# Kernel tuning notes

Hardware: AMD Instinct MI355X
Metric: run time of the kernel (lower is better)

Reference implementation:

```python
import jax, jax.numpy as jnp
import numpy as np

# Forest of complete L-ary trees, BFS level-contiguous node numbering.
B_TREES, ARITY, DEPTH = 8, 4, 8
C, M, NGEN = 8, 100, 4
COUNTS = [B_TREES * ARITY**l for l in range(DEPTH + 1)]
OFFS = np.concatenate([[0], np.cumsum(COUNTS)]).astype(np.int64)
DIM = int(OFFS[-1])  # 699048
# tree id of each node: within-level index // (ARITY**level)
BATCH = np.concatenate([np.arange(COUNTS[l]) // (ARITY**l) for l in range(DEPTH + 1)])


def setup_inputs() -> dict:
    key = jax.random.key(0)
    k1, k2, k3, k4 = jax.random.split(key, 4)
    return {
        "x": jax.random.randint(k1, (DIM,), 0, M, dtype=jnp.int32),
        "A": jax.random.normal(k2, (C, C, ARITY, NGEN), dtype=jnp.float32) * 2.5,
        "B_emit": jax.random.normal(k3, (C, M, NGEN), dtype=jnp.float32) * 2.5,
        "Pi": jax.random.normal(k4, (C, NGEN), dtype=jnp.float32) * 2.5,
    }


def _htmm_loglik(x, A, B_emit, Pi):
    # softmax reparameterization (matches F.softmax axes in torch code)
    smA = jax.nn.softmax(A, axis=0)            # [C,C,L,G], over child state
    smA_t = jnp.transpose(smA, (2, 0, 1, 3))   # [L,C,C,G]
    smB = jax.nn.softmax(B_emit, axis=1)       # [C,M,G]
    smPi = jax.nn.softmax(Pi, axis=0)          # [C,G]

    # preliminary downward: prior state distribution per node, level by level.
    # Children of a parent are contiguous with sibling position j = idx % ARITY.
    prior_lvls = [jnp.broadcast_to(smPi, (COUNTS[0], C, NGEN))]
    for l in range(1, DEPTH + 1):
        n_pa = COUNTS[l - 1]
        # prior_child[c] = sum_d A[c, d, pos_j, g] * prior_pa[d]
        pl = jnp.einsum('jcdg,pdg->pjcg', smA_t, prior_lvls[-1])
        prior_lvls.append(pl.reshape(n_pa * ARITY, C, NGEN))
    prior = jnp.concatenate(prior_lvls, axis=0)  # [DIM,C,G]

    em = jnp.transpose(smB[:, x], (1, 0, 2))     # [DIM,C,G]
    beta0 = prior * em

    ll = jnp.zeros((DIM, NGEN), dtype=beta0.dtype)
    # leaves = deepest level
    beta_lvl = beta0[OFFS[DEPTH]:OFFS[DEPTH + 1]]
    nu = beta_lvl.sum(1)                          # [n_leaves,G]
    beta_lvl = beta_lvl / nu[:, None, :]
    ll = ll.at[OFFS[DEPTH]:OFFS[DEPTH + 1]].set(jnp.log(nu))

    # upward recursion, bottom-up
    for l in range(DEPTH, 0, -1):
        n_pa = COUNTS[l - 1]
        ratio = (beta_lvl / prior[OFFS[l]:OFFS[l + 1]]).reshape(n_pa, ARITY, C, NGEN)
        # beta_uv[d] = sum_c A[c, d, pos_j, g] * beta_ch[c] / prior_ch[c]
        beta_uv = jnp.einsum('jcdg,pjcg->pjdg', smA_t, ratio)  # [n_pa,L,C,G]
        beta_pa = beta0[OFFS[l - 1]:OFFS[l]] * jnp.prod(beta_uv, axis=1)
        nu = beta_pa.sum(1)
        beta_lvl = beta_pa / nu[:, None, :]
        ll = ll.at[OFFS[l - 1]:OFFS[l]].set(jnp.log(nu))

    # scatter per-node log-likelihood contributions into per-tree totals
    return jax.ops.segment_sum(ll, jnp.asarray(BATCH), num_segments=B_TREES)  # [B_TREES,G]


def reference(x, A, B_emit, Pi):
    return _htmm_loglik(x, A, B_emit, Pi)
```

## Files before the change

### kernel.cpp

```cpp
#include <hip/hip_runtime.h>

constexpr int OFFS1 = 8, OFFS2 = 40, OFFS3 = 168, OFFS4 = 680;
constexpr int OFFS5 = 2728, OFFS6 = 10920, OFFS7 = 43688, OFFS8 = 174760;


#define AG_ST(p, v) __hip_atomic_store((p), (v), __ATOMIC_RELAXED, __HIP_MEMORY_SCOPE_AGENT)
#define AG_LD(p) __hip_atomic_load((p), __ATOMIC_RELAXED, __HIP_MEMORY_SCOPE_AGENT)

template <int CTRL>
static __device__ __forceinline__ float dppmov(float v) {
  return __int_as_float(__builtin_amdgcn_update_dpp(0, __float_as_int(v), CTRL, 0xF, 0xF, true));
}

static __device__ __forceinline__ float bfly8(float v) {
  v += dppmov<0xB1>(v);
  v += dppmov<0x4E>(v);
  v += dppmov<0x141>(v);
  return v;
}

static __device__ __forceinline__ void oct8(float v, float pv[8]) {
  float m = dppmov<0x141>(v);
  pv[0] = dppmov<0x00>(v); pv[1] = dppmov<0x55>(v);
  pv[2] = dppmov<0xAA>(v); pv[3] = dppmov<0xFF>(v);
  pv[4] = dppmov<0x00>(m); pv[5] = dppmov<0x55>(m);
  pv[6] = dppmov<0xAA>(m); pv[7] = dppmov<0xFF>(m);
}

static __device__ __forceinline__ float dot8(const float w[8], const float v[8]) {
  return w[0]*v[0] + w[1]*v[1] + w[2]*v[2] + w[3]*v[3] +
         w[4]*v[4] + w[5]*v[5] + w[6]*v[6] + w[7]*v[7];
}

static __device__ __forceinline__ void ld8(const float* p, float pv[8]) {
  const float4* q = (const float4*)p;
  float4 a = q[0], b = q[1];
  pv[0] = a.x; pv[1] = a.y; pv[2] = a.z; pv[3] = a.w;
  pv[4] = b.x; pv[5] = b.y; pv[6] = b.z; pv[7] = b.w;
}

static __device__ __forceinline__ void ld8p(const float* p, float wp[8], int h) {
  const float4* q = (const float4*)p;
  float4 a = q[h], b = q[1 - h];
  wp[0] = a.x; wp[1] = a.y; wp[2] = a.z; wp[3] = a.w;
  wp[4] = b.w; wp[5] = b.z; wp[6] = b.y; wp[7] = b.x;
}

static __device__ __forceinline__ float dot8p(const float wp[8], const float* p, int h) {
  const float4* q = (const float4*)p;
  float4 a = q[h], b = q[1 - h];
  return wp[0]*a.x + wp[1]*a.y + wp[2]*a.z + wp[3]*a.w +
         wp[4]*b.w + wp[5]*b.z + wp[6]*b.y + wp[7]*b.x;
}

static __device__ __forceinline__ float dot8r(const float w[8], const float* p) {
  const float4* q = (const float4*)p;
  float4 a = q[0], b = q[1];
  return w[0]*a.x + w[1]*a.y + w[2]*a.z + w[3]*a.w +
         w[4]*b.x + w[5]*b.y + w[6]*b.z + w[7]*b.w;
}

static __device__ __forceinline__ float rcpf(float x) { return __builtin_amdgcn_rcpf(x); }

static __device__ __forceinline__ float step_down(const float* wtd_l, float v, int j,
                                                  int r, int h) {
  const float* wb = &wtd_l[j * 256 + r];
  float w[8];
#pragma unroll
  for (int k = 0; k < 4; k++) {
    w[k]     = wb[(4 * h + k) * 32];
    w[4 + k] = wb[(7 - 4 * h - k) * 32];
  }
  float pv[8];
  oct8(v, pv);
  return dot8(w, pv);
}

__global__ __launch_bounds__(256) void k_all(const int* __restrict__ x,
                                             const float* __restrict__ A,
                                             const float* __restrict__ Bm,
                                             const float* __restrict__ Pi,
                                             float* __restrict__ RAT4,
                                             float* __restrict__ blocksum,
                                             unsigned* __restrict__ ctr,
                                             float* __restrict__ out) {
  __shared__ __align__(16) float wtd_l[1024];
  __shared__ __align__(16) float emt_l[3200];
  __shared__ __align__(16) float pit_l[32];
  __shared__ __align__(16) float etab_l[12800];
  __shared__ __align__(16) float shbuf[2304];
  __shared__ __align__(16) float rat5buf[16][32];
  __shared__ __align__(16) float pri4buf[4][32];
  __shared__ float llb[4];
  __shared__ int lastf;

  int t = threadIdx.x;
  int r = t & 31, g = r >> 3, s = r & 7, grp = t >> 5;
  int h = s >> 2;
  int b = blockIdx.x, tree = b >> 6;

  if (t < 128) {
    int d = t >> 4, j = (t >> 2) & 3, gg = t & 3;
    float v[8], sum = 0.f;
#pragma unroll
    for (int ss = 0; ss < 8; ss++) { v[ss] = __expf(A[((ss * 8 + d) * 4 + j) * 4 + gg]); sum += v[ss]; }
    float inv = rcpf(sum);
#pragma unroll
    for (int ss = 0; ss < 8; ss++) wtd_l[(j * 8 + d) * 32 + gg * 8 + ss] = v[ss] * inv;
  }
  if (t < 4) {
    float v[8], sum = 0.f;
#pragma unroll
    for (int c = 0; c < 8; c++) { v[c] = __expf(Pi[c * 4 + t]); sum += v[c]; }
    float inv = rcpf(sum);
#pragma unroll
    for (int c = 0; c < 8; c++) pit_l[t * 8 + c] = v[c] * inv;
    llb[t] = 0.f;
  }
  {
    int row = t >> 3, part = t & 7, c = row >> 2, gg = row & 3;
    int m0 = part < 4 ? part * 13 : 52 + (part - 4) * 12;
    int mn = part < 4 ? 13 : 12;
    float sum = 0.f;
    for (int m = m0; m < m0 + mn; m++) sum += __expf(Bm[(c * 100 + m) * 4 + gg]);
    sum = bfly8(sum);
    float inv = rcpf(sum);
    for (int m = m0; m < m0 + mn; m++)
      emt_l[m * 32 + gg * 8 + c] = __expf(Bm[(c * 100 + m) * 4 + gg]) * inv;
  }
  __syncthreads();
  {
    int c7 = t & 127, half = t >> 7;
    int j = c7 >> 5, d = (c7 >> 2) & 7, gg = c7 & 3;
    float w[8];
    ld8(&wtd_l[(j * 8 + d) * 32 + gg * 8], w);
    for (int m = half * 50; m < half * 50 + 50; m++)
      etab_l[(m * 4 + j) * 32 + gg * 8 + d] = dot8r(w, &emt_l[m * 32 + gg * 8]);
  }
  float wtd_p[4][8], wup_p[4][8];
#pragma unroll
  for (int j = 0; j < 4; j++) {
    const float* wb = &wtd_l[j * 256 + r];
#pragma unroll
    for (int k = 0; k < 4; k++) {
      wtd_p[j][k]     = wb[(4 * h + k) * 32];
      wtd_p[j][4 + k] = wb[(7 - 4 * h - k) * 32];
    }
    ld8p(&wtd_l[(j * 8 + s) * 32 + g * 8], wup_p[j], h);
  }
  __syncthreads();

  float acc = 0.f;
#pragma unroll 1
  for (int round = 0; round < 2; round++) {
    int n5 = b * 16 + round * 8 + grp;

    const int4* x8v = (const int4*)(x + OFFS8 + n5 * 64);
    const int4* x7p = (const int4*)(x + OFFS7 + n5 * 16);
    int4 x6v = *(const int4*)(x + OFFS6 + n5 * 4);
    int x5s = x[OFFS5 + n5];
    const int* x6a = (const int*)&x6v;
    int4 x7q[4];
#pragma unroll
    for (int q = 0; q < 4; q++) x7q[q] = x7p[q];
    int4 xls[4][4];
#pragma unroll
    for (int q = 0; q < 4; q++) xls[0][q] = x8v[q];

    float v5 = pit_l[r], pri4 = 0.f;
#pragma unroll
    for (int k = 1; k <= 5; k++) {
      int j = (n5 >> (2 * (5 - k))) & 3;
      v5 = step_down(wtd_l, v5, j, r, h);
      if (k == 4) pri4 = v5;
    }
    float pv5[8];
    oct8(v5, pv5);

    float rat6[4];
#pragma unroll
    for (int q6 = 0; q6 < 4; q6++) {
      if (q6 < 3) {
#pragma unroll
        for (int q = 0; q < 4; q++) xls[q6 + 1][q] = x8v[(q6 + 1) * 4 + q];
      }
      float u6 = dot8(wtd_p[q6], pv5);
      float pv6[8];
      oct8(u6, pv6);
      const int* x7a = (const int*)&x7q[q6];

      float Ep[4][4];
#pragma unroll
      for (int q7 = 0; q7 < 4; q7++) {
        const int* xla = (const int*)&xls[q6][q7];
#pragma unroll
        for (int j = 0; j < 4; j++) Ep[q7][j] = etab_l[(xla[j] * 4 + j) * 32 + r];
      }

      float rat7[4];
#pragma unroll
      for (int q7 = 0; q7 < 4; q7++) {
        float u7 = dot8(wtd_p[q7], pv6);
        float n0 = bfly8(u7 * Ep[q7][0]);
        float n1 = bfly8(u7 * Ep[q7][1]);
        float n2 = bfly8(u7 * Ep[q7][2]);
        float n3 = bfly8(u7 * Ep[q7][3]);
        float p01 = n0 * n1, p23 = n2 * n3;
        float prod = (Ep[q7][0] * Ep[q7][1] * rcpf(p01)) * (Ep[q7][2] * Ep[q7][3] * rcpf(p23));
        acc += __logf(p01) + __logf(p23);
        float em = emt_l[x7a[q7] * 32 + r];
        float nu7 = bfly8(u7 * em * prod);
        acc += __logf(nu7);
        rat7[q7] = em * prod * rcpf(nu7);
      }
      float prod6 = 1.f;
#pragma unroll
      for (int j = 0; j < 4; j++) {
        float pr[8];
        oct8(rat7[j], pr);
        prod6 *= dot8(wup_p[j], pr);
      }
      float em6 = emt_l[x6a[q6] * 32 + r];
      float nu6 = bfly8(u6 * em6 * prod6);
      acc += __logf(nu6);
      rat6[q6] = em6 * prod6 * rcpf(nu6);
    }
    {
      float prod5 = 1.f;
#pragma unroll
      for (int j = 0; j < 4; j++) {
        float pr[8];
        oct8(rat6[j], pr);
        prod5 *= dot8(wup_p[j], pr);
      }
      float em5 = emt_l[x5s * 32 + r];
      float nu5 = bfly8(v5 * em5 * prod5);
      acc += __logf(nu5);
      rat5buf[round * 8 + grp][r] = em5 * prod5 * rcpf(nu5);
    }
    if ((grp & 3) == 0) pri4buf[round * 2 + (grp >> 2)][r] = pri4;
  }
  __syncthreads();

  if (grp < 4) {
    int n4 = b * 4 + grp;
    float prod = 1.f;
#pragma unroll
    for (int j = 0; j < 4; j++) prod *= dot8p(wup_p[j], &rat5buf[grp * 4 + j][g * 8], h);
    float em = emt_l[x[OFFS4 + n4] * 32 + r];
    float pr4 = pri4buf[grp][r];
    float nu = bfly8(pr4 * em * prod);
    acc += __logf(nu);
    AG_ST(&RAT4[n4 * 32 + r], em * prod * rcpf(nu));
  }

  if (s == 0) atomicAdd(&llb[g], acc);
  __syncthreads();
  if (t < 4) AG_ST(&blocksum[b * 4 + t], llb[t]);
  asm volatile("s_waitcnt vmcnt(0)" ::: "memory");
  __syncthreads();
  if (t == 0) {
    unsigned old = __hip_atomic_fetch_add(&ctr[tree * 32], 1u, __ATOMIC_RELAXED,
                                          __HIP_MEMORY_SCOPE_AGENT);
    lastf = (old == 63u || old == 0xAAAAAAE9u) ? 1 : 0;
  }
  __syncthreads();
  if (!lastf) return;

  float* rat4_l = etab_l;
#pragma unroll
  for (int ib = 0; ib < 4; ib++) {
    float tmp[8];
#pragma unroll
    for (int i = 0; i < 8; i++) tmp[i] = AG_LD(&RAT4[tree * 8192 + (ib * 8 + i) * 256 + t]);
#pragma unroll
    for (int i = 0; i < 8; i++) rat4_l[(ib * 8 + i) * 256 + t] = tmp[i];
  }
  if (t < 4) llb[t] = 0.f;
  __syncthreads();

  float* st = &shbuf[grp * 288];
  float acc2 = 0.f;
#pragma unroll 1
  for (int ii = 0; ii < 2; ii++) {
    int l2 = ii * 8 + grp;
    int n2g = tree * 16 + l2;
    float v2 = pit_l[r];
    v2 = step_down(wtd_l, v2, (n2g >> 2) & 3, r, h);
    v2 = step_down(wtd_l, v2, n2g & 3, r, h);
    float pv2[8];
    oct8(v2, pv2);
    float rat3[4];
#pragma unroll
    for (int j3 = 0; j3 < 4; j3++) {
      int n3g = n2g * 4 + j3;
      int i3l = l2 * 4 + j3;
      float p3 = dot8(wtd_p[j3], pv2);
      float prod = 1.f;
#pragma unroll
      for (int j = 0; j < 4; j++) prod *= dot8p(wup_p[j], &rat4_l[(i3l * 4 + j) * 32 + g * 8], h);
      float em = emt_l[x[OFFS3 + n3g] * 32 + r];
      float nu = bfly8(p3 * em * prod);
      acc2 += __logf(nu);
      rat3[j3] = em * prod * rcpf(nu);
    }
    float prod = 1.f;
#pragma unroll
    for (int j = 0; j < 4; j++) {
      float pr[8];
      oct8(rat3[j], pr);
      prod *= dot8(wup_p[j], pr);
    }
    float em = emt_l[x[OFFS2 + n2g] * 32 + r];
    float nu = bfly8(v2 * em * prod);
    acc2 += __logf(nu);
    st[(5 + ii) * 32 + r] = em * prod * rcpf(nu);
  }
  __syncthreads();
  if (grp < 4) {
    int n1g = tree * 4 + grp;
    float pv[8];
    ld8(pit_l + g * 8, pv);
    float v1 = 0.f;
#pragma unroll
    for (int d = 0; d < 8; d++) v1 += wtd_l[(grp * 8 + d) * 32 + r] * pv[d];
    float prod = 1.f;
#pragma unroll
    for (int j = 0; j < 4; j++) {
      int l2 = grp * 4 + j;
      prod *= dot8p(wup_p[j], &shbuf[(l2 & 7) * 288 + (5 + (l2 >> 3)) * 32 + g * 8], h);
    }
    float em = emt_l[x[OFFS1 + n1g] * 32 + r];
    float nu = bfly8(v1 * em * prod);
    acc2 += __logf(nu);
    st[7 * 32 + r] = em * prod * rcpf(nu);
  }
  __syncthreads();
  if (grp == 0) {
    float pr = pit_l[r];
    float prod = 1.f;
#pragma unroll
    for (int j = 0; j < 4; j++) prod *= dot8p(wup_p[j], &shbuf[j * 288 + 7 * 32 + g * 8], h);
    float em = emt_l[x[tree] * 32 + r];
    float nu = bfly8(pr * em * prod);
    acc2 += __logf(nu);
  }
  __syncthreads();
  if (s == 0) atomicAdd(&llb[g], acc2);
  float v = AG_LD(&blocksum[tree * 256 + t]);
  __syncthreads();
  shbuf[t] = v;
  __syncthreads();
#pragma unroll
  for (int off = 128; off >= 4; off >>= 1) {
    if (t < off) shbuf[t] += shbuf[t + off];
    __syncthreads();
  }
  if (t < 4) out[tree * 4 + t] = shbuf[t] + llb[t];
}

extern "C" void kernel_launch(void* const* d_in, const int* in_sizes, int n_in,
                              void* d_out, int out_size, void* d_ws, size_t ws_size,
                              hipStream_t stream) {
  const int* x = (const int*)d_in[0];
  const float* A = (const float*)d_in[1];
  const float* Bm = (const float*)d_in[2];
  const float* Pi = (const float*)d_in[3];
  float* ws = (float*)d_ws;
  unsigned* ctr = (unsigned*)d_ws;
  float* blocksum = ws + 256;
  float* RAT4 = ws + 256 + 2048;
  float* out = (float*)d_out;

  k_all<<<512, 256, 0, stream>>>(x, A, Bm, Pi, RAT4, blocksum, ctr, out);
}
```

Measured before the change: 105.8 us.

## Shrink LDS footprint, drop precomputed emission table, double grid size

Removes the 12800-float etab table and computes leaf emission-transition products on the fly from emt_l. It also adds a transposed weight table so the preloaded wtd_p registers are no longer needed. With the smaller shared memory and launch_bounds(256,4), more blocks can be resident. The grid doubles to 1024 blocks, each handling one round of 8 level-5 subtrees, and the last-block reduction is adjusted to match (128 blocks per tree, two-phase staging of RAT4). The cost is extra per-leaf dot products in exchange for higher occupancy and parallelism.

```diff
diff --git a/kernel.cpp b/kernel.cpp
--- a/kernel.cpp
+++ b/kernel.cpp
@@ -32,13 +32,6 @@
          w[4]*v[4] + w[5]*v[5] + w[6]*v[6] + w[7]*v[7];
 }
 
-static __device__ __forceinline__ void ld8(const float* p, float pv[8]) {
-  const float4* q = (const float4*)p;
-  float4 a = q[0], b = q[1];
-  pv[0] = a.x; pv[1] = a.y; pv[2] = a.z; pv[3] = a.w;
-  pv[4] = b.x; pv[5] = b.y; pv[6] = b.z; pv[7] = b.w;
-}
-
 static __device__ __forceinline__ void ld8p(const float* p, float wp[8], int h) {
   const float4* q = (const float4*)p;
   float4 a = q[h], b = q[1 - h];
@@ -53,51 +46,61 @@
          wp[4]*b.w + wp[5]*b.z + wp[6]*b.y + wp[7]*b.x;
 }
 
-static __device__ __forceinline__ float dot8r(const float w[8], const float* p) {
-  const float4* q = (const float4*)p;
-  float4 a = q[0], b = q[1];
-  return w[0]*a.x + w[1]*a.y + w[2]*a.z + w[3]*a.w +
-         w[4]*b.x + w[5]*b.y + w[6]*b.z + w[7]*b.w;
-}
-
 static __device__ __forceinline__ float rcpf(float x) { return __builtin_amdgcn_rcpf(x); }
 
-static __device__ __forceinline__ float step_down(const float* wtd_l, float v, int j,
-                                                  int r, int h) {
-  const float* wb = &wtd_l[j * 256 + r];
-  float w[8];
-#pragma unroll
-  for (int k = 0; k < 4; k++) {
-    w[k]     = wb[(4 * h + k) * 32];
-    w[4 + k] = wb[(7 - 4 * h - k) * 32];
-  }
+static __device__ __forceinline__ float step_down(const float* wtdT, float v, int j,
+                                                  int sg, int h) {
   float pv[8];
   oct8(v, pv);
-  return dot8(w, pv);
-}
-
-__global__ __launch_bounds__(256) void k_all(const int* __restrict__ x,
-                                             const float* __restrict__ A,
-                                             const float* __restrict__ Bm,
-                                             const float* __restrict__ Pi,
-                                             float* __restrict__ RAT4,
-                                             float* __restrict__ blocksum,
-                                             unsigned* __restrict__ ctr,
-                                             float* __restrict__ out) {
+  return dot8p(pv, &wtdT[(j * 32 + sg) * 8], h);
+}
+
+static __device__ __forceinline__ float upprod(const float wup_p[4][8], const float rat[4]) {
+  float prod = 1.f;
+#pragma unroll
+  for (int j = 0; j < 4; j++) {
+    float pr[8];
+    oct8(rat[j], pr);
+    prod *= dot8(wup_p[j], pr);
+  }
+  return prod;
+}
+
+static __device__ __forceinline__ float leaf7(float u7, float e0, float e1, float e2,
+                                              float e3, float em, float* acc) {
+  float n0 = bfly8(u7 * e0), n1 = bfly8(u7 * e1);
+  float n2 = bfly8(u7 * e2), n3 = bfly8(u7 * e3);
+  float p01 = n0 * n1, p23 = n2 * n3;
+  float prod = (e0 * e1 * rcpf(p01)) * (e2 * e3 * rcpf(p23));
+  *acc += __logf(p01) + __logf(p23);
+  float nu7 = bfly8(u7 * em * prod);
+  *acc += __logf(nu7);
+  return em * prod * rcpf(nu7);
+}
+
+__global__ __launch_bounds__(256, 4) void k_all(const int* __restrict__ x,
+                                                const float* __restrict__ A,
+                                                const float* __restrict__ Bm,
+                                                const float* __restrict__ Pi,
+                                                float* __restrict__ RAT4,
+                                                float* __restrict__ blocksum,
+                                                unsigned* __restrict__ ctr,
+                                                float* __restrict__ out) {
   __shared__ __align__(16) float wtd_l[1024];
+  __shared__ __align__(16) float wtdT[1024];
   __shared__ __align__(16) float emt_l[3200];
   __shared__ __align__(16) float pit_l[32];
-  __shared__ __align__(16) float etab_l[12800];
-  __shared__ __align__(16) float shbuf[2304];
-  __shared__ __align__(16) float rat5buf[16][32];
-  __shared__ __align__(16) float pri4buf[4][32];
+  __shared__ __align__(16) float xb[640];
+  __shared__ __align__(16) float stg[4096];
   __shared__ float llb[4];
   __shared__ int lastf;
 
   int t = threadIdx.x;
   int r = t & 31, g = r >> 3, s = r & 7, grp = t >> 5;
   int h = s >> 2;
-  int b = blockIdx.x, tree = b >> 6;
+  int gb = g * 8;
+  int sg = s * 4 + g;
+  int b = blockIdx.x, tree = b >> 7;
 
   if (t < 128) {
     int d = t >> 4, j = (t >> 2) & 3, gg = t & 3;
@@ -129,49 +132,29 @@
       emt_l[m * 32 + gg * 8 + c] = __expf(Bm[(c * 100 + m) * 4 + gg]) * inv;
   }
   __syncthreads();
+  if (t < 128) {
+    int j = t >> 5, ss = (t >> 2) & 7, gg = t & 3;
+#pragma unroll
+    for (int d = 0; d < 8; d++) wtdT[t * 8 + d] = wtd_l[(j * 8 + d) * 32 + gg * 8 + ss];
+  }
+  float wup_p[4][8];
+#pragma unroll
+  for (int j = 0; j < 4; j++) ld8p(&wtd_l[(j * 8 + s) * 32 + gb], wup_p[j], h);
+  __syncthreads();
+
+  float acc = 0.f;
   {
-    int c7 = t & 127, half = t >> 7;
-    int j = c7 >> 5, d = (c7 >> 2) & 7, gg = c7 & 3;
-    float w[8];
-    ld8(&wtd_l[(j * 8 + d) * 32 + gg * 8], w);
-    for (int m = half * 50; m < half * 50 + 50; m++)
-      etab_l[(m * 4 + j) * 32 + gg * 8 + d] = dot8r(w, &emt_l[m * 32 + gg * 8]);
-  }
-  float wtd_p[4][8], wup_p[4][8];
-#pragma unroll
-  for (int j = 0; j < 4; j++) {
-    const float* wb = &wtd_l[j * 256 + r];
-#pragma unroll
-    for (int k = 0; k < 4; k++) {
-      wtd_p[j][k]     = wb[(4 * h + k) * 32];
-      wtd_p[j][4 + k] = wb[(7 - 4 * h - k) * 32];
-    }
-    ld8p(&wtd_l[(j * 8 + s) * 32 + g * 8], wup_p[j], h);
-  }
-  __syncthreads();
-
-  float acc = 0.f;
-#pragma unroll 1
-  for (int round = 0; round < 2; round++) {
-    int n5 = b * 16 + round * 8 + grp;
-
+    int n5 = b * 8 + grp;
     const int4* x8v = (const int4*)(x + OFFS8 + n5 * 64);
     const int4* x7p = (const int4*)(x + OFFS7 + n5 * 16);
     int4 x6v = *(const int4*)(x + OFFS6 + n5 * 4);
     int x5s = x[OFFS5 + n5];
     const int* x6a = (const int*)&x6v;
-    int4 x7q[4];
-#pragma unroll
-    for (int q = 0; q < 4; q++) x7q[q] = x7p[q];
-    int4 xls[4][4];
-#pragma unroll
-    for (int q = 0; q < 4; q++) xls[0][q] = x8v[q];
 
     float v5 = pit_l[r], pri4 = 0.f;
 #pragma unroll
     for (int k = 1; k <= 5; k++) {
-      int j = (n5 >> (2 * (5 - k))) & 3;
-      v5 = step_down(wtd_l, v5, j, r, h);
+      v5 = step_down(wtdT, v5, (n5 >> (2 * (5 - k))) & 3, sg, h);
       if (k == 4) pri4 = v5;
     }
     float pv5[8];
@@ -180,75 +163,45 @@
     float rat6[4];
 #pragma unroll
     for (int q6 = 0; q6 < 4; q6++) {
-      if (q6 < 3) {
-#pragma unroll
-        for (int q = 0; q < 4; q++) xls[q6 + 1][q] = x8v[(q6 + 1) * 4 + q];
-      }
-      float u6 = dot8(wtd_p[q6], pv5);
+      float u6 = dot8p(pv5, &wtdT[(q6 * 32 + sg) * 8], h);
       float pv6[8];
       oct8(u6, pv6);
-      const int* x7a = (const int*)&x7q[q6];
-
-      float Ep[4][4];
+      int4 x7q = x7p[q6];
+      const int* x7a = (const int*)&x7q;
+
+      float rat7[4];
 #pragma unroll
       for (int q7 = 0; q7 < 4; q7++) {
-        const int* xla = (const int*)&xls[q6][q7];
-#pragma unroll
-        for (int j = 0; j < 4; j++) Ep[q7][j] = etab_l[(xla[j] * 4 + j) * 32 + r];
+        int4 xl = x8v[q6 * 4 + q7];
+        const int* xa = (const int*)&xl;
+        float E[4];
+#pragma unroll
+        for (int j = 0; j < 4; j++) E[j] = dot8p(wup_p[j], &emt_l[xa[j] * 32 + gb], h);
+        float u7 = dot8p(pv6, &wtdT[(q7 * 32 + sg) * 8], h);
+        rat7[q7] = leaf7(u7, E[0], E[1], E[2], E[3], emt_l[x7a[q7] * 32 + r], &acc);
       }
-
-      float rat7[4];
-#pragma unroll
-      for (int q7 = 0; q7 < 4; q7++) {
-        float u7 = dot8(wtd_p[q7], pv6);
-        float n0 = bfly8(u7 * Ep[q7][0]);
-        float n1 = bfly8(u7 * Ep[q7][1]);
-        float n2 = bfly8(u7 * Ep[q7][2]);
-        float n3 = bfly8(u7 * Ep[q7][3]);
-        float p01 = n0 * n1, p23 = n2 * n3;
-        float prod = (Ep[q7][0] * Ep[q7][1] * rcpf(p01)) * (Ep[q7][2] * Ep[q7][3] * rcpf(p23));
-        acc += __logf(p01) + __logf(p23);
-        float em = emt_l[x7a[q7] * 32 + r];
-        float nu7 = bfly8(u7 * em * prod);
-        acc += __logf(nu7);
-        rat7[q7] = em * prod * rcpf(nu7);
-      }
-      float prod6 = 1.f;
-#pragma unroll
-      for (int j = 0; j < 4; j++) {
-        float pr[8];
-        oct8(rat7[j], pr);
-        prod6 *= dot8(wup_p[j], pr);
-      }
+      float prod6 = upprod(wup_p, rat7);
       float em6 = emt_l[x6a[q6] * 32 + r];
       float nu6 = bfly8(u6 * em6 * prod6);
       acc += __logf(nu6);
       rat6[q6] = em6 * prod6 * rcpf(nu6);
     }
-    {
-      float prod5 = 1.f;
-#pragma unroll
-      for (int j = 0; j < 4; j++) {
-        float pr[8];
-        oct8(rat6[j], pr);
-        prod5 *= dot8(wup_p[j], pr);
-      }
-      float em5 = emt_l[x5s * 32 + r];
-      float nu5 = bfly8(v5 * em5 * prod5);
-      acc += __logf(nu5);
-      rat5buf[round * 8 + grp][r] = em5 * prod5 * rcpf(nu5);
-    }
-    if ((grp & 3) == 0) pri4buf[round * 2 + (grp >> 2)][r] = pri4;
-  }
-  __syncthreads();
-
-  if (grp < 4) {
-    int n4 = b * 4 + grp;
+    float prod5 = upprod(wup_p, rat6);
+    float em5 = emt_l[x5s * 32 + r];
+    float nu5 = bfly8(v5 * em5 * prod5);
+    acc += __logf(nu5);
+    xb[grp * 32 + r] = em5 * prod5 * rcpf(nu5);
+    if ((grp & 3) == 0) xb[256 + (grp >> 2) * 32 + r] = pri4;
+  }
+  __syncthreads();
+
+  if (grp < 2) {
+    int n4 = b * 2 + grp;
     float prod = 1.f;
 #pragma unroll
-    for (int j = 0; j < 4; j++) prod *= dot8p(wup_p[j], &rat5buf[grp * 4 + j][g * 8], h);
+    for (int j = 0; j < 4; j++) prod *= dot8p(wup_p[j], &xb[(grp * 4 + j) * 32 + gb], h);
     float em = emt_l[x[OFFS4 + n4] * 32 + r];
-    float pr4 = pri4buf[grp][r];
+    float pr4 = xb[256 + grp * 32 + r];
     float nu = bfly8(pr4 * em * prod);
     acc += __logf(nu);
     AG_ST(&RAT4[n4 * 32 + r], em * prod * rcpf(nu));
@@ -262,101 +215,118 @@
   if (t == 0) {
     unsigned old = __hip_atomic_fetch_add(&ctr[tree * 32], 1u, __ATOMIC_RELAXED,
                                           __HIP_MEMORY_SCOPE_AGENT);
-    lastf = (old == 63u || old == 0xAAAAAAE9u) ? 1 : 0;
+    lastf = (old == 127u || old == 0xAAAAAB29u) ? 1 : 0;
   }
   __syncthreads();
   if (!lastf) return;
 
-  float* rat4_l = etab_l;
-#pragma unroll
-  for (int ib = 0; ib < 4; ib++) {
-    float tmp[8];
-#pragma unroll
-    for (int i = 0; i < 8; i++) tmp[i] = AG_LD(&RAT4[tree * 8192 + (ib * 8 + i) * 256 + t]);
-#pragma unroll
-    for (int i = 0; i < 8; i++) rat4_l[(ib * 8 + i) * 256 + t] = tmp[i];
-  }
+  float tmpA[16], tmpB[16];
+#pragma unroll
+  for (int i = 0; i < 16; i++) tmpA[i] = AG_LD(&RAT4[tree * 8192 + i * 256 + t]);
+#pragma unroll
+  for (int i = 0; i < 16; i++) stg[i * 256 + t] = tmpA[i];
+#pragma unroll
+  for (int i = 0; i < 16; i++) tmpB[i] = AG_LD(&RAT4[tree * 8192 + 4096 + i * 256 + t]);
   if (t < 4) llb[t] = 0.f;
   __syncthreads();
 
-  float* st = &shbuf[grp * 288];
   float acc2 = 0.f;
-#pragma unroll 1
-  for (int ii = 0; ii < 2; ii++) {
-    int l2 = ii * 8 + grp;
-    int n2g = tree * 16 + l2;
+  {
+    int n2A = tree * 16 + grp;
+    int4 x3A = *(const int4*)(x + OFFS3 + n2A * 4);
+    int x2A = x[OFFS2 + n2A];
+    const int* xa = (const int*)&x3A;
     float v2 = pit_l[r];
-    v2 = step_down(wtd_l, v2, (n2g >> 2) & 3, r, h);
-    v2 = step_down(wtd_l, v2, n2g & 3, r, h);
+    v2 = step_down(wtdT, v2, (n2A >> 2) & 3, sg, h);
+    v2 = step_down(wtdT, v2, n2A & 3, sg, h);
     float pv2[8];
     oct8(v2, pv2);
     float rat3[4];
 #pragma unroll
     for (int j3 = 0; j3 < 4; j3++) {
-      int n3g = n2g * 4 + j3;
-      int i3l = l2 * 4 + j3;
-      float p3 = dot8(wtd_p[j3], pv2);
+      float p3 = dot8p(pv2, &wtdT[(j3 * 32 + sg) * 8], h);
       float prod = 1.f;
 #pragma unroll
-      for (int j = 0; j < 4; j++) prod *= dot8p(wup_p[j], &rat4_l[(i3l * 4 + j) * 32 + g * 8], h);
-      float em = emt_l[x[OFFS3 + n3g] * 32 + r];
+      for (int j = 0; j < 4; j++)
+        prod *= dot8p(wup_p[j], &stg[(grp * 16 + j3 * 4 + j) * 32 + gb], h);
+      float em = emt_l[xa[j3] * 32 + r];
       float nu = bfly8(p3 * em * prod);
       acc2 += __logf(nu);
       rat3[j3] = em * prod * rcpf(nu);
     }
-    float prod = 1.f;
-#pragma unroll
-    for (int j = 0; j < 4; j++) {
-      float pr[8];
-      oct8(rat3[j], pr);
-      prod *= dot8(wup_p[j], pr);
-    }
-    float em = emt_l[x[OFFS2 + n2g] * 32 + r];
+    float prod = upprod(wup_p, rat3);
+    float em = emt_l[x2A * 32 + r];
     float nu = bfly8(v2 * em * prod);
     acc2 += __logf(nu);
-    st[(5 + ii) * 32 + r] = em * prod * rcpf(nu);
+    xb[grp * 32 + r] = em * prod * rcpf(nu);
+  }
+  __syncthreads();
+#pragma unroll
+  for (int i = 0; i < 16; i++) stg[i * 256 + t] = tmpB[i];
+  __syncthreads();
+  {
+    int n2B = tree * 16 + 8 + grp;
+    int4 x3B = *(const int4*)(x + OFFS3 + n2B * 4);
+    int x2B = x[OFFS2 + n2B];
+    const int* xb3 = (const int*)&x3B;
+    float v2 = pit_l[r];
+    v2 = step_down(wtdT, v2, (n2B >> 2) & 3, sg, h);
+    v2 = step_down(wtdT, v2, n2B & 3, sg, h);
+    float pv2[8];
+    oct8(v2, pv2);
+    float rat3[4];
+#pragma unroll
+    for (int j3 = 0; j3 < 4; j3++) {
+      float p3 = dot8p(pv2, &wtdT[(j3 * 32 + sg) * 8], h);
+      float prod = 1.f;
+#pragma unroll
+      for (int j = 0; j < 4; j++)
+        prod *= dot8p(wup_p[j], &stg[(grp * 16 + j3 * 4 + j) * 32 + gb], h);
+      float em = emt_l[xb3[j3] * 32 + r];
+      float nu = bfly8(p3 * em * prod);
+      acc2 += __logf(nu);
+      rat3[j3] = em * prod * rcpf(nu);
+    }
+    float prod = upprod(wup_p, rat3);
+    float em = emt_l[x2B * 32 + r];
+    float nu = bfly8(v2 * em * prod);
+    acc2 += __logf(nu);
+    xb[(8 + grp) * 32 + r] = em * prod * rcpf(nu);
   }
   __syncthreads();
   if (grp < 4) {
     int n1g = tree * 4 + grp;
-    float pv[8];
-    ld8(pit_l + g * 8, pv);
-    float v1 = 0.f;
-#pragma unroll
-    for (int d = 0; d < 8; d++) v1 += wtd_l[(grp * 8 + d) * 32 + r] * pv[d];
+    float v1 = step_down(wtdT, pit_l[r], grp, sg, h);
     float prod = 1.f;
 #pragma unroll
-    for (int j = 0; j < 4; j++) {
-      int l2 = grp * 4 + j;
-      prod *= dot8p(wup_p[j], &shbuf[(l2 & 7) * 288 + (5 + (l2 >> 3)) * 32 + g * 8], h);
-    }
+    for (int j = 0; j < 4; j++) prod *= dot8p(wup_p[j], &xb[(grp * 4 + j) * 32 + gb], h);
     float em = emt_l[x[OFFS1 + n1g] * 32 + r];
     float nu = bfly8(v1 * em * prod);
     acc2 += __logf(nu);
-    st[7 * 32 + r] = em * prod * rcpf(nu);
+    xb[512 + grp * 32 + r] = em * prod * rcpf(nu);
   }
   __syncthreads();
   if (grp == 0) {
     float pr = pit_l[r];
     float prod = 1.f;
 #pragma unroll
-    for (int j = 0; j < 4; j++) prod *= dot8p(wup_p[j], &shbuf[j * 288 + 7 * 32 + g * 8], h);
+    for (int j = 0; j < 4; j++) prod *= dot8p(wup_p[j], &xb[512 + j * 32 + gb], h);
     float em = emt_l[x[tree] * 32 + r];
     float nu = bfly8(pr * em * prod);
     acc2 += __logf(nu);
   }
   __syncthreads();
   if (s == 0) atomicAdd(&llb[g], acc2);
-  float v = AG_LD(&blocksum[tree * 256 + t]);
-  __syncthreads();
-  shbuf[t] = v;
+  float v = AG_LD(&blocksum[tree * 512 + t]) + AG_LD(&blocksum[tree * 512 + 256 + t]);
+  __syncthreads();
+  stg[t] = v;
   __syncthreads();
 #pragma unroll
   for (int off = 128; off >= 4; off >>= 1) {
-    if (t < off) shbuf[t] += shbuf[t + off];
+    if (t < off) stg[t] += stg[t + off];
     __syncthreads();
   }
-  if (t < 4) out[tree * 4 + t] = shbuf[t] + llb[t];
+  if (t < 4) out[tree * 4 + t] = stg[t] + llb[t];
 }
 
 extern "C" void kernel_launch(void* const* d_in, const int* in_sizes, int n_in,
@@ -369,8 +339,8 @@
   float* ws = (float*)d_ws;
   unsigned* ctr = (unsigned*)d_ws;
   float* blocksum = ws + 256;
-  float* RAT4 = ws + 256 + 2048;
+  float* RAT4 = ws + 256 + 4096;
   float* out = (float*)d_out;
 
-  k_all<<<512, 256, 0, stream>>>(x, A, Bm, Pi, RAT4, blocksum, ctr, out);
-}
+  k_all<<<1024, 256, 0, stream>>>(x, A, Bm, Pi, RAT4, blocksum, ctr, out);
+}
```

Measured after the change: 141.2 us. 33.4% more time.
